# Kernel optimization log

Hardware: AMD Instinct MI355X
Metric: run time of the kernel (lower is better)

Reference implementation:

```python
import jax, jax.numpy as jnp
import numpy as np

CHUNK = 128  # chunk size for the causal linear-attention recurrence
EPS = 1e-10


def _causal_numerator(q, k, v, chunk=CHUNK):
    """N_i = sum_{j<=i} (q_i . k_j) v_j, computed chunk-recurrently.

    q,k: [B,H,N,D]; v: [B,H,N,E] -> [B,H,N,E]
    """
    B, H, N, D = q.shape
    E = v.shape[-1]
    nc = N // chunk
    qc = jnp.moveaxis(q.reshape(B, H, nc, chunk, D), 2, 0)  # [nc,B,H,c,D]
    kc = jnp.moveaxis(k.reshape(B, H, nc, chunk, D), 2, 0)
    vc = jnp.moveaxis(v.reshape(B, H, nc, chunk, E), 2, 0)
    mask = jnp.tril(jnp.ones((chunk, chunk), dtype=q.dtype))  # causal within chunk

    def step(S, inp):  # S: running sum of k_j (outer) v_j -> [B,H,D,E]
        qi, ki, vi = inp
        scores = jnp.einsum('bhid,bhjd->bhij', qi, ki) * mask
        intra = jnp.einsum('bhij,bhje->bhie', scores, vi)
        inter = jnp.einsum('bhid,bhde->bhie', qi, S)
        S = S + jnp.einsum('bhjd,bhje->bhde', ki, vi)
        return S, intra + inter

    S0 = jnp.zeros((B, H, D, E), q.dtype)
    _, outs = jax.lax.scan(step, S0, (qc, kc, vc))  # [nc,B,H,c,E]
    return jnp.moveaxis(outs, 0, 2).reshape(B, H, N, E)


def _causal_denominator(q, k):
    # D_i = q_i . cumsum_j<=i k_j  -> [B,H,N]
    return jnp.einsum('bhnd,bhnd->bhn', q, jnp.cumsum(k, axis=-2))


def setup_inputs() -> dict:
    key = jax.random.key(0)
    ks = jax.random.split(key, 5)
    shape = (2, 8, 4096, 64)
    names = ['q', 'k', 'q_rot', 'k_rot', 'v']
    # feature-mapped inputs (Performer softmax features) are positive
    return {n: jax.random.uniform(ks[i], shape, dtype=jnp.float32) for i, n in enumerate(names)}


def reference(q, k, q_rot, k_rot, v):
    N = _causal_numerator(q, k, v) + _causal_numerator(q_rot, k_rot, v)
    D = _causal_denominator(q, k) + _causal_denominator(q_rot, k_rot)
    return N * (1.0 / (D + EPS))[..., None]
```

## Files before the change

### kernel.cpp

```cpp
#include <hip/hip_runtime.h>

#define SEQ 4096
#define DIM 64
#define CHUNK 128
#define NC 32
#define EPSV 1e-10f
#define KS_OFF 2097152

typedef __attribute__((ext_vector_type(8))) short s16x8;
typedef __attribute__((ext_vector_type(4))) float f32x4;

__device__ __forceinline__ unsigned short f2bf(float f) {
  unsigned int u = __float_as_uint(f);
  u += 0x7FFF + ((u >> 16) & 1);
  return (unsigned short)(u >> 16);
}
__device__ __forceinline__ float bf2f_lo(unsigned int x) { return __uint_as_float(x << 16); }

__device__ __forceinline__ unsigned int cvtpk(float lo, float hi) {
  unsigned int r;
  asm("v_cvt_pk_bf16_f32 %0, %1, %2" : "=v"(r) : "v"(lo), "v"(hi));
  return r;
}
__device__ __forceinline__ s16x8 pack8(float4 a, float4 b) {
  union { unsigned int u[4]; s16x8 v; } r;
  r.u[0] = cvtpk(a.x, a.y); r.u[1] = cvtpk(a.z, a.w);
  r.u[2] = cvtpk(b.x, b.y); r.u[3] = cvtpk(b.z, b.w);
  return r.v;
}

template<bool SUM, int TPB>
__device__ __forceinline__ float gather_T(const float* __restrict__ gp,
                                          unsigned short* __restrict__ dst, int t) {
  int d = t & 63, grp = t >> 6;
  constexpr int GRPS = TPB / 64;
  constexpr int NI = 16 / GRPS;
  float s = 0.f;
#pragma unroll
  for (int i = 0; i < NI; ++i) {
    int j8 = grp + i * GRPS;
    const float* p = gp + (size_t)(j8 * 8) * DIM + d;
    float x[8];
#pragma unroll
    for (int u2 = 0; u2 < 8; ++u2) x[u2] = p[(size_t)u2 * DIM];
    if (SUM) {
#pragma unroll
      for (int u2 = 0; u2 < 8; ++u2) s += x[u2];
    }
    union { unsigned int u4[4]; s16x8 v; } seg;
#pragma unroll
    for (int u2 = 0; u2 < 4; ++u2) seg.u4[u2] = cvtpk(x[2 * u2], x[2 * u2 + 1]);
    *(s16x8*)&dst[d * 136 + j8 * 8] = seg.v;
  }
  return s;
}

__global__ __launch_bounds__(256) void pass_a(const float* __restrict__ k0,
                                              const float* __restrict__ k1,
                                              const float* __restrict__ v,
                                              float* __restrict__ ws) {
  __shared__ __align__(16) unsigned short skT[64 * 136];
  __shared__ __align__(16) unsigned short svT[64 * 136];
  __shared__ float spart[4][64];
  int bid = blockIdx.x;
  int m = bid >> 9, rem = bid & 511, hh = rem >> 5, c = rem & 31;
  const float* kp = (m ? k1 : k0) + (size_t)hh * SEQ * DIM + (size_t)c * CHUNK * DIM;
  const float* vp = v + (size_t)hh * SEQ * DIM + (size_t)c * CHUNK * DIM;
  int t = threadIdx.x;

  float s = gather_T<true, 256>(kp, skT, t);
  gather_T<false, 256>(vp, svT, t);
  spart[t >> 6][t & 63] = s;
  __syncthreads();

  if (t < 64)
    ws[KS_OFF + (size_t)bid * 64 + t] = spart[0][t] + spart[1][t] + spart[2][t] + spart[3][t];

  int w = t >> 6, L = t & 63, g = L >> 4, cL = L & 15;
  f32x4 acc[4];
#pragma unroll
  for (int ct = 0; ct < 4; ++ct) acc[ct] = (f32x4){0.f, 0.f, 0.f, 0.f};
#pragma unroll
  for (int ks = 0; ks < 4; ++ks) {
    s16x8 aF = *(const s16x8*)&svT[(w * 16 + cL) * 136 + ks * 32 + g * 8];
#pragma unroll
    for (int ct = 0; ct < 4; ++ct) {
      s16x8 bF = *(const s16x8*)&skT[(ct * 16 + cL) * 136 + ks * 32 + g * 8];
      acc[ct] = __builtin_amdgcn_mfma_f32_16x16x32_bf16(aF, bF, acc[ct], 0, 0, 0);
    }
  }
  unsigned short* Sp = (unsigned short*)ws + (size_t)bid * 4096;
#pragma unroll
  for (int ct = 0; ct < 4; ++ct)
#pragma unroll
    for (int r = 0; r < 4; ++r)
      Sp[(size_t)(w * 16 + g * 4 + r) * 64 + ct * 16 + cL] = f2bf(acc[ct][r]);
}

__global__ __launch_bounds__(256) void pass_b(float* __restrict__ ws) {
  int t = threadIdx.x;
  if (blockIdx.x < 256) {
    int gid = blockIdx.x * 256 + t;
    int mh = gid >> 11, de2 = gid & 2047;
    unsigned int* p = (unsigned int*)ws + (size_t)mh * NC * 2048 + de2;
    unsigned int x[NC];
#pragma unroll
    for (int c = 0; c < NC; ++c) x[c] = p[(size_t)c * 2048];
    float r0 = 0.f, r1 = 0.f;
#pragma unroll
    for (int c = 0; c < NC; ++c) {
      unsigned int xc = x[c];
      p[(size_t)c * 2048] = (unsigned int)f2bf(r0) | ((unsigned int)f2bf(r1) << 16);
      r0 += bf2f_lo(xc & 0xFFFFu);
      r1 += __uint_as_float(xc & 0xFFFF0000u);
    }
  } else {
    int gid = (blockIdx.x - 256) * 256 + t;
    int mh = gid >> 6, d = gid & 63;
    float* p = ws + KS_OFF + (size_t)mh * NC * 64 + d;
    float x[NC];
#pragma unroll
    for (int c = 0; c < NC; ++c) x[c] = p[(size_t)c * 64];
    float run = 0.f;
#pragma unroll
    for (int c = 0; c < NC; ++c) {
      p[(size_t)c * 64] = run;
      run += x[c];
    }
  }
}

__global__ __launch_bounds__(512, 4) void pass_c(const float* __restrict__ q0,
                                                 const float* __restrict__ q1,
                                                 const float* __restrict__ k0,
                                                 const float* __restrict__ k1,
                                                 const float* __restrict__ v,
                                                 const float* __restrict__ ws,
                                                 float* __restrict__ out) {
  __shared__ __align__(16) unsigned short svT[64 * 136];
  __shared__ __align__(16) union UBuf {
    struct {
      unsigned short sST[2][64 * 72];
      float skpref[2][64];
    } a;
    float exch[128 * 66];
  } u;
  __shared__ float sden[2][128];

  int hh = blockIdx.x >> 5, c = blockIdx.x & 31;
  int t = threadIdx.x;
  int w = t >> 6, L = t & 63, g = L >> 4, cL = L & 15;
  size_t off = (size_t)hh * SEQ * DIM + (size_t)c * CHUNK * DIM;
  const int rtS0 = w, rtS1 = 7 - w;

  gather_T<false, 512>(v + off, svT, t);

  {
    int half = t >> 8, tt = t & 255;
    const unsigned short* Sp = (const unsigned short*)ws + (size_t)(half * 512 + hh * 32 + c) * 4096;
    const float* Kp = ws + KS_OFF + (size_t)(half * 512 + hh * 32 + c) * 64;
#pragma unroll
    for (int p2 = 0; p2 < 2; ++p2) {
      int idx = tt + p2 * 256;
      *(s16x8*)&u.a.sST[half][(idx >> 3) * 72 + (idx & 7) * 8] = *(const s16x8*)&Sp[idx * 8];
    }
    if (tt < 64) u.a.skpref[half][tt] = Kp[tt];
  }
  __syncthreads();

  f32x4 accO[2][4];
#pragma unroll
  for (int a = 0; a < 2; ++a)
#pragma unroll
    for (int b = 0; b < 4; ++b) accO[a][b] = (f32x4){0.f, 0.f, 0.f, 0.f};
  float dent[2] = {0.f, 0.f};
  s16x8 aq[2][2];

#pragma unroll
  for (int s2 = 0; s2 < 2; ++s2) {
    int rt = s2 ? rtS1 : rtS0;
    const float* qp = (s2 ? q1 : q0) + off;
    int row = rt * 16 + cL;
#pragma unroll
    for (int h = 0; h < 2; ++h) {
      const float* qb = qp + (size_t)row * DIM + h * 32 + g * 8;
      float4 a0 = *(const float4*)qb;
      float4 a1 = *(const float4*)(qb + 4);
      const float* kq = &u.a.skpref[s2][h * 32 + g * 8];
      dent[s2] += a0.x * kq[0] + a0.y * kq[1] + a0.z * kq[2] + a0.w * kq[3]
                + a1.x * kq[4] + a1.y * kq[5] + a1.z * kq[6] + a1.w * kq[7];
      aq[s2][h] = pack8(a0, a1);
    }
#pragma unroll
    for (int h = 0; h < 2; ++h)
#pragma unroll
      for (int et = 0; et < 4; ++et) {
        s16x8 bS = *(const s16x8*)&u.a.sST[s2][(et * 16 + cL) * 72 + h * 32 + g * 8];
        accO[s2][et] = __builtin_amdgcn_mfma_f32_16x16x32_bf16(aq[s2][h], bS, accO[s2][et], 0, 0, 0);
      }
  }

  {
    int srcA = cL + ((g & 1) << 5), srcB = srcA + 16;
    bool hiG = g >= 2;
#pragma unroll
    for (int s2 = 0; s2 < 2; ++s2) {
      int rt = s2 ? rtS1 : rtS0;
      const float* kp = (s2 ? k1 : k0) + off;
      for (int ks = 0; ks <= (rt >> 1); ++ks) {
        unsigned int E0e, E1e;
        {
          int jt = 2 * ks;
          const float* kb = kp + (size_t)(jt * 16 + cL) * DIM;
          float4 b0 = *(const float4*)(kb + g * 8);
          float4 b1 = *(const float4*)(kb + g * 8 + 4);
          float4 b2 = *(const float4*)(kb + 32 + g * 8);
          float4 b3 = *(const float4*)(kb + 32 + g * 8 + 4);
          s16x8 kf0 = pack8(b0, b1), kf1 = pack8(b2, b3);
          f32x4 C = (f32x4){0.f, 0.f, 0.f, 0.f};
          C = __builtin_amdgcn_mfma_f32_16x16x32_bf16(kf0, aq[s2][0], C, 0, 0, 0);
          C = __builtin_amdgcn_mfma_f32_16x16x32_bf16(kf1, aq[s2][1], C, 0, 0, 0);
          if (jt == rt) {
#pragma unroll
            for (int r = 0; r < 4; ++r)
              if (g * 4 + r > cL) C[r] = 0.f;
          }
          dent[s2] += C[0] + C[1] + C[2] + C[3];
          E0e = cvtpk(C[0], C[1]); E1e = cvtpk(C[2], C[3]);
        }
        int S0o = 0, S1o = 0, S2o = 0, S3o = 0;
        if (2 * ks + 1 <= rt) {
          int jt = 2 * ks + 1;
          const float* kb = kp + (size_t)(jt * 16 + cL) * DIM;
          float4 b0 = *(const float4*)(kb + g * 8);
          float4 b1 = *(const float4*)(kb + g * 8 + 4);
          float4 b2 = *(const float4*)(kb + 32 + g * 8);
          float4 b3 = *(const float4*)(kb + 32 + g * 8 + 4);
          s16x8 kf0 = pack8(b0, b1), kf1 = pack8(b2, b3);
          f32x4 C = (f32x4){0.f, 0.f, 0.f, 0.f};
          C = __builtin_amdgcn_mfma_f32_16x16x32_bf16(kf0, aq[s2][0], C, 0, 0, 0);
          C = __builtin_amdgcn_mfma_f32_16x16x32_bf16(kf1, aq[s2][1], C, 0, 0, 0);
          if (jt == rt) {
#pragma unroll
            for (int r = 0; r < 4; ++r)
              if (g * 4 + r > cL) C[r] = 0.f;
          }
          dent[s2] += C[0] + C[1] + C[2] + C[3];
          unsigned int E0o = cvtpk(C[0], C[1]), E1o = cvtpk(C[2], C[3]);
          S0o = __shfl((int)E0o, srcA); S1o = __shfl((int)E1o, srcA);
          S2o = __shfl((int)E0o, srcB); S3o = __shfl((int)E1o, srcB);
        }
        int S0e = __shfl((int)E0e, srcA); int S1e = __shfl((int)E1e, srcA);
        int S2e = __shfl((int)E0e, srcB); int S3e = __shfl((int)E1e, srcB);
        union { int d4[4]; s16x8 v8; } ap;
        ap.d4[0] = hiG ? S0o : S0e;
        ap.d4[1] = hiG ? S1o : S1e;
        ap.d4[2] = hiG ? S2o : S2e;
        ap.d4[3] = hiG ? S3o : S3e;
#pragma unroll
        for (int et = 0; et < 4; ++et) {
          s16x8 bV = *(const s16x8*)&svT[(et * 16 + cL) * 136 + ks * 32 + g * 8];
          accO[s2][et] = __builtin_amdgcn_mfma_f32_16x16x32_bf16(ap.v8, bV, accO[s2][et], 0, 0, 0);
        }
      }
    }
  }

#pragma unroll
  for (int s2 = 0; s2 < 2; ++s2) {
    float dt = dent[s2];
    dt += __shfl_xor(dt, 16);
    dt += __shfl_xor(dt, 32);
    dent[s2] = dt;
  }
  if (L < 16) {
    sden[0][rtS0 * 16 + L] = dent[0];
    sden[1][rtS1 * 16 + L] = dent[1];
  }
  __syncthreads();

#pragma unroll
  for (int et = 0; et < 4; ++et)
#pragma unroll
    for (int r = 0; r < 4; ++r)
      u.exch[(rtS1 * 16 + g * 4 + r) * 66 + et * 16 + cL] = accO[1][et][r];
  __syncthreads();

  float* op = out + off;
#pragma unroll
  for (int r = 0; r < 4; ++r) {
    int row = rtS0 * 16 + g * 4 + r;
    float inv = 1.f / (sden[0][row] + sden[1][row] + EPSV);
#pragma unroll
    for (int et = 0; et < 4; ++et) {
      float O = accO[0][et][r] + u.exch[row * 66 + et * 16 + cL];
      op[(size_t)row * DIM + et * 16 + cL] = O * inv;
    }
  }
}

extern "C" void kernel_launch(void* const* d_in, const int* in_sizes, int n_in,
                              void* d_out, int out_size, void* d_ws, size_t ws_size,
                              hipStream_t stream) {
  const float* q  = (const float*)d_in[0];
  const float* k  = (const float*)d_in[1];
  const float* qr = (const float*)d_in[2];
  const float* kr = (const float*)d_in[3];
  const float* v  = (const float*)d_in[4];
  float* out = (float*)d_out;
  float* ws  = (float*)d_ws;

  hipLaunchKernelGGL(pass_a, dim3(1024), dim3(256), 0, stream, k, kr, v, ws);
  hipLaunchKernelGGL(pass_b, dim3(264), dim3(256), 0, stream, ws);
  hipLaunchKernelGGL(pass_c, dim3(512), dim3(512), 0, stream, q, qr, k, kr, v, ws, out);
}
```

Baseline: 139.6 us.

## Drop prefix-scan kernel; compute chunk prefix sums in pass_c and merge pass_a halves

Removes the separate pass_b scan kernel. pass_c now sums the per-chunk bf16 states of all preceding chunks directly from the workspace, and does the same for the key sums. pass_a is merged so that one 512-thread block handles both k and k_rot for a chunk, which loads v only once. Both kernels use a swizzled block index so that blocks for the same head are spread across the grid. This saves a kernel launch and a read-write round trip through the workspace. In exchange, pass_c does O(c) redundant reads per block, which makes work uneven across chunks, and the prefix is summed in fp32 from bf16 values rather than being a sequentially rounded scan.

```diff
diff --git a/kernel.cpp b/kernel.cpp
--- a/kernel.cpp
+++ b/kernel.cpp
@@ -15,7 +15,6 @@
   u += 0x7FFF + ((u >> 16) & 1);
   return (unsigned short)(u >> 16);
 }
-__device__ __forceinline__ float bf2f_lo(unsigned int x) { return __uint_as_float(x << 16); }
 
 __device__ __forceinline__ unsigned int cvtpk(float lo, float hi) {
   unsigned int r;
@@ -28,6 +27,8 @@
   r.u[2] = cvtpk(b.x, b.y); r.u[3] = cvtpk(b.z, b.w);
   return r.v;
 }
+
+__device__ __forceinline__ int swz512(int b) { return ((b & 7) << 6) | (b >> 3); }
 
 template<bool SUM, int TPB>
 __device__ __forceinline__ float gather_T(const float* __restrict__ gp,
@@ -55,79 +56,48 @@
   return s;
 }
 
-__global__ __launch_bounds__(256) void pass_a(const float* __restrict__ k0,
-                                              const float* __restrict__ k1,
-                                              const float* __restrict__ v,
-                                              float* __restrict__ ws) {
-  __shared__ __align__(16) unsigned short skT[64 * 136];
+__global__ __launch_bounds__(512, 4) void pass_a(const float* __restrict__ k0,
+                                                 const float* __restrict__ k1,
+                                                 const float* __restrict__ v,
+                                                 float* __restrict__ ws) {
+  __shared__ __align__(16) unsigned short skT[2][64 * 136];
   __shared__ __align__(16) unsigned short svT[64 * 136];
-  __shared__ float spart[4][64];
-  int bid = blockIdx.x;
-  int m = bid >> 9, rem = bid & 511, hh = rem >> 5, c = rem & 31;
-  const float* kp = (m ? k1 : k0) + (size_t)hh * SEQ * DIM + (size_t)c * CHUNK * DIM;
-  const float* vp = v + (size_t)hh * SEQ * DIM + (size_t)c * CHUNK * DIM;
-  int t = threadIdx.x;
-
-  float s = gather_T<true, 256>(kp, skT, t);
-  gather_T<false, 256>(vp, svT, t);
-  spart[t >> 6][t & 63] = s;
+  __shared__ float spart[2][4][64];
+  int bid = swz512(blockIdx.x);
+  int hh = bid >> 5, c = bid & 31;
+  int t = threadIdx.x, half = t >> 8, tt = t & 255;
+  size_t off = (size_t)hh * SEQ * DIM + (size_t)c * CHUNK * DIM;
+  const float* kp = (half ? k1 : k0) + off;
+  int chunk = half * 512 + hh * 32 + c;
+
+  float s = gather_T<true, 256>(kp, skT[half], tt);
+  gather_T<false, 512>(v + off, svT, t);
+  spart[half][tt >> 6][tt & 63] = s;
   __syncthreads();
 
-  if (t < 64)
-    ws[KS_OFF + (size_t)bid * 64 + t] = spart[0][t] + spart[1][t] + spart[2][t] + spart[3][t];
-
-  int w = t >> 6, L = t & 63, g = L >> 4, cL = L & 15;
+  if (tt < 64)
+    ws[KS_OFF + (size_t)chunk * 64 + tt] = spart[half][0][tt] + spart[half][1][tt]
+                                         + spart[half][2][tt] + spart[half][3][tt];
+
+  int wv = tt >> 6, L = tt & 63, g = L >> 4, cL = L & 15;
   f32x4 acc[4];
 #pragma unroll
   for (int ct = 0; ct < 4; ++ct) acc[ct] = (f32x4){0.f, 0.f, 0.f, 0.f};
 #pragma unroll
   for (int ks = 0; ks < 4; ++ks) {
-    s16x8 aF = *(const s16x8*)&svT[(w * 16 + cL) * 136 + ks * 32 + g * 8];
+    s16x8 aF = *(const s16x8*)&svT[(wv * 16 + cL) * 136 + ks * 32 + g * 8];
 #pragma unroll
     for (int ct = 0; ct < 4; ++ct) {
-      s16x8 bF = *(const s16x8*)&skT[(ct * 16 + cL) * 136 + ks * 32 + g * 8];
+      s16x8 bF = *(const s16x8*)&skT[half][(ct * 16 + cL) * 136 + ks * 32 + g * 8];
       acc[ct] = __builtin_amdgcn_mfma_f32_16x16x32_bf16(aF, bF, acc[ct], 0, 0, 0);
     }
   }
-  unsigned short* Sp = (unsigned short*)ws + (size_t)bid * 4096;
+  unsigned short* Sp = (unsigned short*)ws + (size_t)chunk * 4096;
 #pragma unroll
   for (int ct = 0; ct < 4; ++ct)
 #pragma unroll
     for (int r = 0; r < 4; ++r)
-      Sp[(size_t)(w * 16 + g * 4 + r) * 64 + ct * 16 + cL] = f2bf(acc[ct][r]);
-}
-
-__global__ __launch_bounds__(256) void pass_b(float* __restrict__ ws) {
-  int t = threadIdx.x;
-  if (blockIdx.x < 256) {
-    int gid = blockIdx.x * 256 + t;
-    int mh = gid >> 11, de2 = gid & 2047;
-    unsigned int* p = (unsigned int*)ws + (size_t)mh * NC * 2048 + de2;
-    unsigned int x[NC];
-#pragma unroll
-    for (int c = 0; c < NC; ++c) x[c] = p[(size_t)c * 2048];
-    float r0 = 0.f, r1 = 0.f;
-#pragma unroll
-    for (int c = 0; c < NC; ++c) {
-      unsigned int xc = x[c];
-      p[(size_t)c * 2048] = (unsigned int)f2bf(r0) | ((unsigned int)f2bf(r1) << 16);
-      r0 += bf2f_lo(xc & 0xFFFFu);
-      r1 += __uint_as_float(xc & 0xFFFF0000u);
-    }
-  } else {
-    int gid = (blockIdx.x - 256) * 256 + t;
-    int mh = gid >> 6, d = gid & 63;
-    float* p = ws + KS_OFF + (size_t)mh * NC * 64 + d;
-    float x[NC];
-#pragma unroll
-    for (int c = 0; c < NC; ++c) x[c] = p[(size_t)c * 64];
-    float run = 0.f;
-#pragma unroll
-    for (int c = 0; c < NC; ++c) {
-      p[(size_t)c * 64] = run;
-      run += x[c];
-    }
-  }
+      Sp[(size_t)(wv * 16 + g * 4 + r) * 64 + ct * 16 + cL] = f2bf(acc[ct][r]);
 }
 
 __global__ __launch_bounds__(512, 4) void pass_c(const float* __restrict__ q0,
@@ -147,24 +117,48 @@
   } u;
   __shared__ float sden[2][128];
 
-  int hh = blockIdx.x >> 5, c = blockIdx.x & 31;
+  int bid = swz512(blockIdx.x);
+  int hh = bid >> 5, c = bid & 31;
   int t = threadIdx.x;
   int w = t >> 6, L = t & 63, g = L >> 4, cL = L & 15;
+  int half = t >> 8, tt = t & 255;
   size_t off = (size_t)hh * SEQ * DIM + (size_t)c * CHUNK * DIM;
   const int rtS0 = w, rtS1 = 7 - w;
 
   gather_T<false, 512>(v + off, svT, t);
 
   {
-    int half = t >> 8, tt = t & 255;
-    const unsigned short* Sp = (const unsigned short*)ws + (size_t)(half * 512 + hh * 32 + c) * 4096;
-    const float* Kp = ws + KS_OFF + (size_t)(half * 512 + hh * 32 + c) * 64;
-#pragma unroll
-    for (int p2 = 0; p2 < 2; ++p2) {
-      int idx = tt + p2 * 256;
-      *(s16x8*)&u.a.sST[half][(idx >> 3) * 72 + (idx & 7) * 8] = *(const s16x8*)&Sp[idx * 8];
-    }
-    if (tt < 64) u.a.skpref[half][tt] = Kp[tt];
+    int cb = half * 512 + hh * 32;
+    const unsigned int* S32 = (const unsigned int*)ws;
+    float aS[16];
+#pragma unroll
+    for (int i = 0; i < 16; ++i) aS[i] = 0.f;
+    for (int cc = 0; cc < c; ++cc) {
+      const unsigned int* p = S32 + (size_t)(cb + cc) * 2048 + tt * 8;
+      uint4 A = *(const uint4*)p;
+      uint4 B = *(const uint4*)(p + 4);
+      aS[0]  += __uint_as_float(A.x << 16); aS[1]  += __uint_as_float(A.x & 0xFFFF0000u);
+      aS[2]  += __uint_as_float(A.y << 16); aS[3]  += __uint_as_float(A.y & 0xFFFF0000u);
+      aS[4]  += __uint_as_float(A.z << 16); aS[5]  += __uint_as_float(A.z & 0xFFFF0000u);
+      aS[6]  += __uint_as_float(A.w << 16); aS[7]  += __uint_as_float(A.w & 0xFFFF0000u);
+      aS[8]  += __uint_as_float(B.x << 16); aS[9]  += __uint_as_float(B.x & 0xFFFF0000u);
+      aS[10] += __uint_as_float(B.y << 16); aS[11] += __uint_as_float(B.y & 0xFFFF0000u);
+      aS[12] += __uint_as_float(B.z << 16); aS[13] += __uint_as_float(B.z & 0xFFFF0000u);
+      aS[14] += __uint_as_float(B.w << 16); aS[15] += __uint_as_float(B.w & 0xFFFF0000u);
+    }
+    union { unsigned int u4[4]; s16x8 v8; } w0, w1;
+#pragma unroll
+    for (int i = 0; i < 4; ++i) w0.u4[i] = cvtpk(aS[2 * i], aS[2 * i + 1]);
+#pragma unroll
+    for (int i = 0; i < 4; ++i) w1.u4[i] = cvtpk(aS[8 + 2 * i], aS[8 + 2 * i + 1]);
+    int i0 = 2 * tt, i1 = 2 * tt + 1;
+    *(s16x8*)&u.a.sST[half][(i0 >> 3) * 72 + (i0 & 7) * 8] = w0.v8;
+    *(s16x8*)&u.a.sST[half][(i1 >> 3) * 72 + (i1 & 7) * 8] = w1.v8;
+    if (tt < 64) {
+      float run = 0.f;
+      for (int cc = 0; cc < c; ++cc) run += ws[KS_OFF + (size_t)(cb + cc) * 64 + tt];
+      u.a.skpref[half][tt] = run;
+    }
   }
   __syncthreads();
 
@@ -310,7 +304,6 @@
   float* out = (float*)d_out;
   float* ws  = (float*)d_ws;
 
-  hipLaunchKernelGGL(pass_a, dim3(1024), dim3(256), 0, stream, k, kr, v, ws);
-  hipLaunchKernelGGL(pass_b, dim3(264), dim3(256), 0, stream, ws);
+  hipLaunchKernelGGL(pass_a, dim3(512), dim3(512), 0, stream, k, kr, v, ws);
   hipLaunchKernelGGL(pass_c, dim3(512), dim3(512), 0, stream, q, qr, k, kr, v, ws, out);
 }
```

New measurement: 151.3 us. 8.4% more time.

## Stage bf16 copies of k and transposed v in pass_a for pass_c reuse

Applied to the files above, without the earlier changes.

pass_a now writes bf16-packed copies of k and k_rot, plus the already-transposed bf16 v tile, into the workspace. pass_c then reads these compact bf16 buffers instead of re-reading fp32 k/v and converting or transposing them. This halves pass_c's k/v read traffic and removes its gather/transpose work, at the cost of extra writes in pass_a. pass_a also gains a launch_bounds occupancy hint.

```diff
diff --git a/kernel.cpp b/kernel.cpp
--- a/kernel.cpp
+++ b/kernel.cpp
@@ -6,6 +6,8 @@
 #define NC 32
 #define EPSV 1e-10f
 #define KS_OFF 2097152
+#define KB_OFF 2162688
+#define VB_OFF 6356992
 
 typedef __attribute__((ext_vector_type(8))) short s16x8;
 typedef __attribute__((ext_vector_type(4))) float f32x4;
@@ -55,18 +57,20 @@
   return s;
 }
 
-__global__ __launch_bounds__(256) void pass_a(const float* __restrict__ k0,
-                                              const float* __restrict__ k1,
-                                              const float* __restrict__ v,
-                                              float* __restrict__ ws) {
+__global__ __launch_bounds__(256, 4) void pass_a(const float* __restrict__ k0,
+                                                 const float* __restrict__ k1,
+                                                 const float* __restrict__ v,
+                                                 float* __restrict__ ws) {
   __shared__ __align__(16) unsigned short skT[64 * 136];
   __shared__ __align__(16) unsigned short svT[64 * 136];
   __shared__ float spart[4][64];
   int bid = blockIdx.x;
   int m = bid >> 9, rem = bid & 511, hh = rem >> 5, c = rem & 31;
-  const float* kp = (m ? k1 : k0) + (size_t)hh * SEQ * DIM + (size_t)c * CHUNK * DIM;
-  const float* vp = v + (size_t)hh * SEQ * DIM + (size_t)c * CHUNK * DIM;
+  size_t off = (size_t)hh * SEQ * DIM + (size_t)c * CHUNK * DIM;
+  const float* kp = (m ? k1 : k0) + off;
+  const float* vp = v + off;
   int t = threadIdx.x;
+  int chunk = m * 512 + rem;
 
   float s = gather_T<true, 256>(kp, skT, t);
   gather_T<false, 256>(vp, svT, t);
@@ -74,7 +78,7 @@
   __syncthreads();
 
   if (t < 64)
-    ws[KS_OFF + (size_t)bid * 64 + t] = spart[0][t] + spart[1][t] + spart[2][t] + spart[3][t];
+    ws[KS_OFF + (size_t)chunk * 64 + t] = spart[0][t] + spart[1][t] + spart[2][t] + spart[3][t];
 
   int w = t >> 6, L = t & 63, g = L >> 4, cL = L & 15;
   f32x4 acc[4];
@@ -89,12 +93,35 @@
       acc[ct] = __builtin_amdgcn_mfma_f32_16x16x32_bf16(aF, bF, acc[ct], 0, 0, 0);
     }
   }
-  unsigned short* Sp = (unsigned short*)ws + (size_t)bid * 4096;
+  unsigned short* Sp = (unsigned short*)ws + (size_t)chunk * 4096;
 #pragma unroll
   for (int ct = 0; ct < 4; ++ct)
 #pragma unroll
     for (int r = 0; r < 4; ++r)
       Sp[(size_t)(w * 16 + g * 4 + r) * 64 + ct * 16 + cL] = f2bf(acc[ct][r]);
+
+  {
+    unsigned short* kb16 = (unsigned short*)(ws + KB_OFF) + (size_t)chunk * 8192;
+#pragma unroll
+    for (int p2 = 0; p2 < 2; ++p2) {
+      int idx = t + p2 * 256;
+      const float* src = kp + (size_t)idx * 16;
+      float4 x0 = *(const float4*)src;
+      float4 x1 = *(const float4*)(src + 4);
+      float4 x2 = *(const float4*)(src + 8);
+      float4 x3 = *(const float4*)(src + 12);
+      *(s16x8*)&kb16[(size_t)idx * 16] = pack8(x0, x1);
+      *(s16x8*)&kb16[(size_t)idx * 16 + 8] = pack8(x2, x3);
+    }
+  }
+  if (m == 0) {
+    unsigned short* vb16 = (unsigned short*)(ws + VB_OFF) + (size_t)rem * 8192;
+#pragma unroll
+    for (int p2 = 0; p2 < 4; ++p2) {
+      int idx = t + p2 * 256;
+      *(s16x8*)&vb16[(size_t)idx * 8] = *(const s16x8*)&svT[(idx >> 4) * 136 + (idx & 15) * 8];
+    }
+  }
 }
 
 __global__ __launch_bounds__(256) void pass_b(float* __restrict__ ws) {
@@ -132,9 +159,6 @@
 
 __global__ __launch_bounds__(512, 4) void pass_c(const float* __restrict__ q0,
                                                  const float* __restrict__ q1,
-                                                 const float* __restrict__ k0,
-                                                 const float* __restrict__ k1,
-                                                 const float* __restrict__ v,
                                                  const float* __restrict__ ws,
                                                  float* __restrict__ out) {
   __shared__ __align__(16) unsigned short svT[64 * 136];
@@ -150,13 +174,19 @@
   int hh = blockIdx.x >> 5, c = blockIdx.x & 31;
   int t = threadIdx.x;
   int w = t >> 6, L = t & 63, g = L >> 4, cL = L & 15;
+  int half = t >> 8, tt = t & 255;
   size_t off = (size_t)hh * SEQ * DIM + (size_t)c * CHUNK * DIM;
   const int rtS0 = w, rtS1 = 7 - w;
 
-  gather_T<false, 512>(v + off, svT, t);
-
   {
-    int half = t >> 8, tt = t & 255;
+    const unsigned short* vb16 = (const unsigned short*)(ws + VB_OFF) + (size_t)(hh * 32 + c) * 8192;
+#pragma unroll
+    for (int p2 = 0; p2 < 2; ++p2) {
+      int idx = t + p2 * 512;
+      *(s16x8*)&svT[(idx >> 4) * 136 + (idx & 15) * 8] = *(const s16x8*)&vb16[(size_t)idx * 8];
+    }
+  }
+  {
     const unsigned short* Sp = (const unsigned short*)ws + (size_t)(half * 512 + hh * 32 + c) * 4096;
     const float* Kp = ws + KS_OFF + (size_t)(half * 512 + hh * 32 + c) * 64;
 #pragma unroll
@@ -206,17 +236,15 @@
 #pragma unroll
     for (int s2 = 0; s2 < 2; ++s2) {
       int rt = s2 ? rtS1 : rtS0;
-      const float* kp = (s2 ? k1 : k0) + off;
+      const unsigned short* kb16 = (const unsigned short*)(ws + KB_OFF)
+                                 + (size_t)(s2 * 512 + hh * 32 + c) * 8192;
       for (int ks = 0; ks <= (rt >> 1); ++ks) {
         unsigned int E0e, E1e;
         {
           int jt = 2 * ks;
-          const float* kb = kp + (size_t)(jt * 16 + cL) * DIM;
-          float4 b0 = *(const float4*)(kb + g * 8);
-          float4 b1 = *(const float4*)(kb + g * 8 + 4);
-          float4 b2 = *(const float4*)(kb + 32 + g * 8);
-          float4 b3 = *(const float4*)(kb + 32 + g * 8 + 4);
-          s16x8 kf0 = pack8(b0, b1), kf1 = pack8(b2, b3);
+          int row = jt * 16 + cL;
+          s16x8 kf0 = *(const s16x8*)&kb16[(size_t)row * 64 + g * 8];
+          s16x8 kf1 = *(const s16x8*)&kb16[(size_t)row * 64 + 32 + g * 8];
           f32x4 C = (f32x4){0.f, 0.f, 0.f, 0.f};
           C = __builtin_amdgcn_mfma_f32_16x16x32_bf16(kf0, aq[s2][0], C, 0, 0, 0);
           C = __builtin_amdgcn_mfma_f32_16x16x32_bf16(kf1, aq[s2][1], C, 0, 0, 0);
@@ -231,12 +259,9 @@
         int S0o = 0, S1o = 0, S2o = 0, S3o = 0;
         if (2 * ks + 1 <= rt) {
           int jt = 2 * ks + 1;
-          const float* kb = kp + (size_t)(jt * 16 + cL) * DIM;
-          float4 b0 = *(const float4*)(kb + g * 8);
-          float4 b1 = *(const float4*)(kb + g * 8 + 4);
-          float4 b2 = *(const float4*)(kb + 32 + g * 8);
-          float4 b3 = *(const float4*)(kb + 32 + g * 8 + 4);
-          s16x8 kf0 = pack8(b0, b1), kf1 = pack8(b2, b3);
+          int row = jt * 16 + cL;
+          s16x8 kf0 = *(const s16x8*)&kb16[(size_t)row * 64 + g * 8];
+          s16x8 kf1 = *(const s16x8*)&kb16[(size_t)row * 64 + 32 + g * 8];
           f32x4 C = (f32x4){0.f, 0.f, 0.f, 0.f};
           C = __builtin_amdgcn_mfma_f32_16x16x32_bf16(kf0, aq[s2][0], C, 0, 0, 0);
           C = __builtin_amdgcn_mfma_f32_16x16x32_bf16(kf1, aq[s2][1], C, 0, 0, 0);
@@ -312,5 +337,5 @@
 
   hipLaunchKernelGGL(pass_a, dim3(1024), dim3(256), 0, stream, k, kr, v, ws);
   hipLaunchKernelGGL(pass_b, dim3(264), dim3(256), 0, stream, ws);
-  hipLaunchKernelGGL(pass_c, dim3(512), dim3(512), 0, stream, q, qr, k, kr, v, ws, out);
-}
+  hipLaunchKernelGGL(pass_c, dim3(512), dim3(512), 0, stream, q, qr, ws, out);
+}
```

Measured after the change: 145.9 us. +4.5%, slower.

## Split pass_c work per row tile so each wave computes both feature maps

Applied to the files above, without the earlier changes.

Pass_c now launches 1024 blocks of 256 threads, up from 512 blocks of 512. Each wave owns one 16-row tile and accumulates both the q/k and q_rot/k_rot contributions into a single accumulator. This removes the LDS exchange buffer, the shared denominator array and two block barriers from the epilogue, replacing them with an in-wave shuffle of the denominator. Row tiles are assigned to balance the causal triangle across waves, and block indices are swizzled so blocks for the same chunk are interleaved. The cost is that each block reloads the V transpose and the S state, which doubles that LDS-fill traffic.

```diff
diff --git a/kernel.cpp b/kernel.cpp
--- a/kernel.cpp
+++ b/kernel.cpp
@@ -130,7 +130,7 @@
   }
 }
 
-__global__ __launch_bounds__(512, 4) void pass_c(const float* __restrict__ q0,
+__global__ __launch_bounds__(256, 4) void pass_c(const float* __restrict__ q0,
                                                  const float* __restrict__ q1,
                                                  const float* __restrict__ k0,
                                                  const float* __restrict__ k1,
@@ -138,47 +138,42 @@
                                                  const float* __restrict__ ws,
                                                  float* __restrict__ out) {
   __shared__ __align__(16) unsigned short svT[64 * 136];
-  __shared__ __align__(16) union UBuf {
-    struct {
-      unsigned short sST[2][64 * 72];
-      float skpref[2][64];
-    } a;
-    float exch[128 * 66];
-  } u;
-  __shared__ float sden[2][128];
-
-  int hh = blockIdx.x >> 5, c = blockIdx.x & 31;
+  __shared__ __align__(16) unsigned short sST[2][64 * 72];
+  __shared__ float skpref[2][64];
+
+  int bidx = blockIdx.x;
+  int x = bidx & 7, rb = bidx >> 3, b = rb & 1, rr = rb >> 1;
+  int ci = x * 64 + rr;
+  int hh = ci >> 5, c = ci & 31;
   int t = threadIdx.x;
   int w = t >> 6, L = t & 63, g = L >> 4, cL = L & 15;
+  int rt = ((w & 2) << 1) | (b ^ (3 * (w & 1)));
   size_t off = (size_t)hh * SEQ * DIM + (size_t)c * CHUNK * DIM;
-  const int rtS0 = w, rtS1 = 7 - w;
-
-  gather_T<false, 512>(v + off, svT, t);
-
-  {
-    int half = t >> 8, tt = t & 255;
-    const unsigned short* Sp = (const unsigned short*)ws + (size_t)(half * 512 + hh * 32 + c) * 4096;
-    const float* Kp = ws + KS_OFF + (size_t)(half * 512 + hh * 32 + c) * 64;
+
+  gather_T<false, 256>(v + off, svT, t);
+#pragma unroll
+  for (int half = 0; half < 2; ++half) {
+    const unsigned short* Sp = (const unsigned short*)ws + (size_t)(half * 512 + ci) * 4096;
 #pragma unroll
     for (int p2 = 0; p2 < 2; ++p2) {
-      int idx = tt + p2 * 256;
-      *(s16x8*)&u.a.sST[half][(idx >> 3) * 72 + (idx & 7) * 8] = *(const s16x8*)&Sp[idx * 8];
-    }
-    if (tt < 64) u.a.skpref[half][tt] = Kp[tt];
+      int idx = t + p2 * 256;
+      *(s16x8*)&sST[half][(idx >> 3) * 72 + (idx & 7) * 8] = *(const s16x8*)&Sp[idx * 8];
+    }
+  }
+  if (t < 64) {
+    skpref[0][t] = ws[KS_OFF + (size_t)ci * 64 + t];
+    skpref[1][t] = ws[KS_OFF + (size_t)(512 + ci) * 64 + t];
   }
   __syncthreads();
 
-  f32x4 accO[2][4];
-#pragma unroll
-  for (int a = 0; a < 2; ++a)
-#pragma unroll
-    for (int b = 0; b < 4; ++b) accO[a][b] = (f32x4){0.f, 0.f, 0.f, 0.f};
-  float dent[2] = {0.f, 0.f};
+  f32x4 accO[4];
+#pragma unroll
+  for (int e2 = 0; e2 < 4; ++e2) accO[e2] = (f32x4){0.f, 0.f, 0.f, 0.f};
+  float dent = 0.f;
   s16x8 aq[2][2];
 
 #pragma unroll
   for (int s2 = 0; s2 < 2; ++s2) {
-    int rt = s2 ? rtS1 : rtS0;
     const float* qp = (s2 ? q1 : q0) + off;
     int row = rt * 16 + cL;
 #pragma unroll
@@ -186,17 +181,17 @@
       const float* qb = qp + (size_t)row * DIM + h * 32 + g * 8;
       float4 a0 = *(const float4*)qb;
       float4 a1 = *(const float4*)(qb + 4);
-      const float* kq = &u.a.skpref[s2][h * 32 + g * 8];
-      dent[s2] += a0.x * kq[0] + a0.y * kq[1] + a0.z * kq[2] + a0.w * kq[3]
-                + a1.x * kq[4] + a1.y * kq[5] + a1.z * kq[6] + a1.w * kq[7];
+      const float* kq = &skpref[s2][h * 32 + g * 8];
+      dent += a0.x * kq[0] + a0.y * kq[1] + a0.z * kq[2] + a0.w * kq[3]
+            + a1.x * kq[4] + a1.y * kq[5] + a1.z * kq[6] + a1.w * kq[7];
       aq[s2][h] = pack8(a0, a1);
     }
 #pragma unroll
     for (int h = 0; h < 2; ++h)
 #pragma unroll
       for (int et = 0; et < 4; ++et) {
-        s16x8 bS = *(const s16x8*)&u.a.sST[s2][(et * 16 + cL) * 72 + h * 32 + g * 8];
-        accO[s2][et] = __builtin_amdgcn_mfma_f32_16x16x32_bf16(aq[s2][h], bS, accO[s2][et], 0, 0, 0);
+        s16x8 bS = *(const s16x8*)&sST[s2][(et * 16 + cL) * 72 + h * 32 + g * 8];
+        accO[et] = __builtin_amdgcn_mfma_f32_16x16x32_bf16(aq[s2][h], bS, accO[et], 0, 0, 0);
       }
   }
 
@@ -205,13 +200,12 @@
     bool hiG = g >= 2;
 #pragma unroll
     for (int s2 = 0; s2 < 2; ++s2) {
-      int rt = s2 ? rtS1 : rtS0;
-      const float* kp = (s2 ? k1 : k0) + off;
+      const float* kpp = (s2 ? k1 : k0) + off;
       for (int ks = 0; ks <= (rt >> 1); ++ks) {
         unsigned int E0e, E1e;
         {
           int jt = 2 * ks;
-          const float* kb = kp + (size_t)(jt * 16 + cL) * DIM;
+          const float* kb = kpp + (size_t)(jt * 16 + cL) * DIM;
           float4 b0 = *(const float4*)(kb + g * 8);
           float4 b1 = *(const float4*)(kb + g * 8 + 4);
           float4 b2 = *(const float4*)(kb + 32 + g * 8);
@@ -225,13 +219,13 @@
             for (int r = 0; r < 4; ++r)
               if (g * 4 + r > cL) C[r] = 0.f;
           }
-          dent[s2] += C[0] + C[1] + C[2] + C[3];
+          dent += C[0] + C[1] + C[2] + C[3];
           E0e = cvtpk(C[0], C[1]); E1e = cvtpk(C[2], C[3]);
         }
         int S0o = 0, S1o = 0, S2o = 0, S3o = 0;
         if (2 * ks + 1 <= rt) {
           int jt = 2 * ks + 1;
-          const float* kb = kp + (size_t)(jt * 16 + cL) * DIM;
+          const float* kb = kpp + (size_t)(jt * 16 + cL) * DIM;
           float4 b0 = *(const float4*)(kb + g * 8);
           float4 b1 = *(const float4*)(kb + g * 8 + 4);
           float4 b2 = *(const float4*)(kb + 32 + g * 8);
@@ -245,7 +239,7 @@
             for (int r = 0; r < 4; ++r)
               if (g * 4 + r > cL) C[r] = 0.f;
           }
-          dent[s2] += C[0] + C[1] + C[2] + C[3];
+          dent += C[0] + C[1] + C[2] + C[3];
           unsigned int E0o = cvtpk(C[0], C[1]), E1o = cvtpk(C[2], C[3]);
           S0o = __shfl((int)E0o, srcA); S1o = __shfl((int)E1o, srcA);
           S2o = __shfl((int)E0o, srcB); S3o = __shfl((int)E1o, srcB);
@@ -260,42 +254,24 @@
 #pragma unroll
         for (int et = 0; et < 4; ++et) {
           s16x8 bV = *(const s16x8*)&svT[(et * 16 + cL) * 136 + ks * 32 + g * 8];
-          accO[s2][et] = __builtin_amdgcn_mfma_f32_16x16x32_bf16(ap.v8, bV, accO[s2][et], 0, 0, 0);
+          accO[et] = __builtin_amdgcn_mfma_f32_16x16x32_bf16(ap.v8, bV, accO[et], 0, 0, 0);
         }
       }
     }
   }
 
-#pragma unroll
-  for (int s2 = 0; s2 < 2; ++s2) {
-    float dt = dent[s2];
-    dt += __shfl_xor(dt, 16);
-    dt += __shfl_xor(dt, 32);
-    dent[s2] = dt;
-  }
-  if (L < 16) {
-    sden[0][rtS0 * 16 + L] = dent[0];
-    sden[1][rtS1 * 16 + L] = dent[1];
-  }
-  __syncthreads();
-
-#pragma unroll
-  for (int et = 0; et < 4; ++et)
-#pragma unroll
-    for (int r = 0; r < 4; ++r)
-      u.exch[(rtS1 * 16 + g * 4 + r) * 66 + et * 16 + cL] = accO[1][et][r];
-  __syncthreads();
+  dent += __shfl_xor(dent, 16);
+  dent += __shfl_xor(dent, 32);
 
   float* op = out + off;
 #pragma unroll
   for (int r = 0; r < 4; ++r) {
-    int row = rtS0 * 16 + g * 4 + r;
-    float inv = 1.f / (sden[0][row] + sden[1][row] + EPSV);
-#pragma unroll
-    for (int et = 0; et < 4; ++et) {
-      float O = accO[0][et][r] + u.exch[row * 66 + et * 16 + cL];
-      op[(size_t)row * DIM + et * 16 + cL] = O * inv;
-    }
+    float dr = __shfl(dent, g * 4 + r);
+    float inv = 1.f / (dr + EPSV);
+    int row = rt * 16 + g * 4 + r;
+#pragma unroll
+    for (int et = 0; et < 4; ++et)
+      op[(size_t)row * DIM + et * 16 + cL] = accO[et][r] * inv;
   }
 }
 
@@ -312,5 +288,5 @@
 
   hipLaunchKernelGGL(pass_a, dim3(1024), dim3(256), 0, stream, k, kr, v, ws);
   hipLaunchKernelGGL(pass_b, dim3(264), dim3(256), 0, stream, ws);
-  hipLaunchKernelGGL(pass_c, dim3(512), dim3(512), 0, stream, q, qr, k, kr, v, ws, out);
-}
+  hipLaunchKernelGGL(pass_c, dim3(1024), dim3(256), 0, stream, q, qr, k, kr, v, ws, out);
+}
```

After: 139.0 us. About the same (-0.4%).
